# Kernel optimization log

Hardware: AMD Instinct MI355X
Metric: run time of the kernel (lower is better)

Reference implementation:

```python
import jax, jax.numpy as jnp
import numpy as np

N_U, N_I, D_IN_U, D_IN_I, D, D_QOL, B = 4096, 4096, 256, 256, 256, 4, 8192

def _w(key, shape, scale=0.05):
    return (jax.random.normal(key, shape) * scale).astype(jnp.float32)

def setup_inputs() -> dict:
    key = jax.random.key(0)
    ks = jax.random.split(key, 24)
    inp = {
        "x_u": jax.random.normal(ks[0], (N_U, D_IN_U), jnp.float32),
        "x_i": jax.random.normal(ks[1], (N_I, D_IN_I), jnp.float32),
        "social_adj": jax.random.randint(ks[2], (N_U, N_U), 0, 2, jnp.int32),
        "ui_adj": jax.random.randint(ks[3], (N_U, N_I), 0, 2, jnp.int32),
        "user_idx": jax.random.randint(ks[4], (B,), 0, N_U, jnp.int32),
        "item_idx": jax.random.randint(ks[5], (B,), 0, N_I, jnp.int32),
        "q_u": jax.random.normal(ks[6], (N_U, D_QOL), jnp.float32),
        # params (Linear stored as [in, out]; y = x @ W + b)
        "user_W": _w(ks[7], (D_IN_U, D)), "user_b": jnp.zeros((D,), jnp.float32),
        "item_W": _w(ks[8], (D_IN_I, D)), "item_b": jnp.zeros((D,), jnp.float32),
        "soc_W": _w(ks[9], (D, D)), "soc_a": _w(ks[10], (2 * D,)),
        "cnt_W": _w(ks[11], (D, D)), "cnt_a": _w(ks[12], (2 * D,)),
        "gate_W": _w(ks[13], (D_QOL, D)), "gate_b": jnp.zeros((D,), jnp.float32),
        "qproj_W": _w(ks[14], (D_QOL, D)), "qproj_b": jnp.zeros((D,), jnp.float32),
        "alpha_q": jnp.float32(0.3),
        "pred_W1": _w(ks[15], (2 * D, D)), "pred_b1": jnp.zeros((D,), jnp.float32),
        "pred_W2": _w(ks[16], (D, 1)), "pred_b2": jnp.zeros((1,), jnp.float32),
    }
    return inp

def _gat(Wh_src, Wh_dst, a, adj):
    """GAT additive attention: src rows attend over dst cols where adj!=0.
    Rows with no neighbors produce zero output (matches nan_to_num + zeroing)."""
    d = Wh_src.shape[-1]
    a1 = Wh_src @ a[:d]          # [N_src]
    a2 = Wh_dst @ a[d:]          # [N_dst]
    e = jax.nn.leaky_relu(a1[:, None] + a2[None, :], 0.2)  # [N_src, N_dst]
    mask = adj != 0
    neg_inf = jnp.float32(-jnp.inf)
    m = jnp.max(jnp.where(mask, e, neg_inf), axis=-1, keepdims=True)
    m = jnp.where(jnp.isfinite(m), m, 0.0)  # guard empty rows
    ex = jnp.where(mask, jnp.exp(e - m), 0.0)
    denom = jnp.sum(ex, axis=-1, keepdims=True)
    alpha = jnp.where(denom > 0, ex / jnp.where(denom > 0, denom, 1.0), 0.0)
    out = alpha @ Wh_dst
    return out, alpha

def reference(x_u, x_i, social_adj, ui_adj, user_idx, item_idx, q_u,
              user_W, user_b, item_W, item_b, soc_W, soc_a, cnt_W, cnt_a,
              gate_W, gate_b, qproj_W, qproj_b, alpha_q,
              pred_W1, pred_b1, pred_W2, pred_b2):
    h_u = x_u @ user_W + user_b               # [N_u, D]
    h_i = x_i @ item_W + item_b               # [N_i, D]
    # social attention (users over users)
    Wh = h_u @ soc_W
    soc_msg, alpha_s = _gat(Wh, Wh, soc_a, social_adj)
    # content attention (users over items)
    Wu = h_u @ cnt_W
    Wi = h_i @ cnt_W
    cnt_msg, alpha_c = _gat(Wu, Wi, cnt_a, ui_adj)
    h_u_out = jax.nn.elu(soc_msg + cnt_msg + h_u)
    # QoL gate
    gate = jax.nn.sigmoid(q_u @ gate_W + gate_b)
    qproj = q_u @ qproj_W + qproj_b
    h_u_out = h_u_out + alpha_q * gate * qproj
    # pair prediction (dropout inactive at eval)
    cat = jnp.concatenate([h_u_out[user_idx], h_i[item_idx]], axis=-1)  # [B, 2D]
    hid = jax.nn.relu(cat @ pred_W1 + pred_b1)
    r = (hid @ pred_W2 + pred_b2)[..., 0]
    r_hat = 1.0 + 4.0 * jax.nn.sigmoid(r)
    return r_hat, alpha_s, alpha_c
```

## Files before the change

### kernel.cpp

```cpp
#include <hip/hip_runtime.h>

typedef unsigned short u16;
typedef unsigned int u32;
typedef unsigned char u8;
typedef unsigned long long u64;
typedef float f32x4 __attribute__((ext_vector_type(4)));
typedef __bf16 bf16x8 __attribute__((ext_vector_type(8)));

#define NU 4096
#define DD 256
#define BB 8192

__device__ inline u16 f2b(float f) {
    u32 u = __builtin_bit_cast(u32, f);
    u32 r = (u + 0x7fffu + ((u >> 16) & 1u)) >> 16;
    return (u16)r;
}
__device__ inline float b2f(u16 v) { return __builtin_bit_cast(float, (u32)v << 16); }
__device__ inline float lrelu(float x) { return x > 0.f ? x : 0.2f * x; }
__device__ inline float decmax(u32 e) {
    return __builtin_bit_cast(float, (e >> 31) ? (e & 0x7fffffffu) : ~e);
}

#define BARRIER_LGKM() asm volatile("s_waitcnt lgkmcnt(0)\ns_barrier" ::: "memory")

__global__ __launch_bounds__(256) void k_pro(
    const float* __restrict__ x_u, const float* __restrict__ x_i,
    const float* __restrict__ user_W, const float* __restrict__ item_W, const float* __restrict__ pred_W1,
    const float* __restrict__ soc_W, const float* __restrict__ soc_a,
    const float* __restrict__ cnt_W, const float* __restrict__ cnt_a,
    const float* __restrict__ user_b, const float* __restrict__ item_b,
    u16* __restrict__ xu_b, u16* __restrict__ xi_b,
    u16* __restrict__ uWt, u16* __restrict__ iWt, u16* __restrict__ p1Wt,
    float* __restrict__ uvec,
    u16* __restrict__ WusT, u16* __restrict__ WicT,
    float* __restrict__ b_us, float* __restrict__ b_ic, u32* __restrict__ MhEnc) {
    __shared__ float t[64][65];
    __shared__ float sa[256];
    const int b = blockIdx.x;
    const int tid = threadIdx.x;

    if (b < 1024) {
        const float* in = (b < 512) ? x_u : x_i;
        u16* out = (b < 512) ? xu_b : xi_b;
        int i = (b & 511) * 256 + tid;
        const float4 v0 = *(const float4*)(in + (size_t)i * 8);
        const float4 v1 = *(const float4*)(in + (size_t)i * 8 + 4);
        u16 u[8] = {f2b(v0.x), f2b(v0.y), f2b(v0.z), f2b(v0.w),
                    f2b(v1.x), f2b(v1.y), f2b(v1.z), f2b(v1.w)};
        *(uint4*)(out + (size_t)i * 8) = *(uint4*)u;
    } else if (b < 1088) {
        int j = b - 1024;
        const float* in;
        u16* out;
        int R;
        if (j < 16) { in = user_W; out = uWt; R = 256; }
        else if (j < 32) { in = item_W; out = iWt; R = 256; j -= 16; }
        else { in = pred_W1; out = p1Wt; R = 512; j -= 32; }
        int rb = (j >> 2) * 64, cb = (j & 3) * 64;
        for (int k = 0; k < 16; ++k) {
            int idx = k * 256 + tid;
            int lr = idx >> 6, lc = idx & 63;
            t[lr][lc] = in[(size_t)(rb + lr) * 256 + cb + lc];
        }
        __syncthreads();
        for (int k = 0; k < 16; ++k) {
            int idx = k * 256 + tid;
            int lr = idx >> 6, lc = idx & 63;
            out[(size_t)(cb + lr) * R + rb + lc] = f2b(t[lc][lr]);
        }
    } else if (b < 1092) {
        int bb = b - 1088;
        if (bb == 0 && tid < 2) MhEnc[tid] = 0u;
        const float* W = (bb < 2) ? soc_W : cnt_W;
        const float* a = ((bb < 2) ? soc_a : cnt_a) + (bb & 1) * 256;
        int lane = tid & 63, wv = tid >> 6;
        sa[tid] = a[tid];
        __syncthreads();
        for (int rr = 0; rr < 64; ++rr) {
            int in = wv * 64 + rr;
            float4 w4 = *(const float4*)(W + (size_t)in * 256 + lane * 4);
            float acc = w4.x * sa[lane * 4] + w4.y * sa[lane * 4 + 1] + w4.z * sa[lane * 4 + 2] + w4.w * sa[lane * 4 + 3];
#pragma unroll
            for (int off = 32; off; off >>= 1) acc += __shfl_down(acc, off);
            if (lane == 0) uvec[bb * 256 + in] = acc;
        }
    } else {
        int j = b - 1092;
        int p = j >> 4;
        int tile = j & 15;
        const float* A = p ? item_W : user_W;
        const float* Bw = p ? cnt_W : soc_W;
        const float* bvec = p ? item_b : user_b;
        u16* outT = p ? WicT : WusT;
        float* outb = p ? b_ic : b_us;
        int m0 = (tile >> 2) * 64, n0 = (tile & 3) * 64;
        int m = m0 + (tid >> 4) * 4, n = n0 + (tid & 15) * 4;
        float acc[4][4];
#pragma unroll
        for (int i = 0; i < 4; ++i)
#pragma unroll
            for (int k = 0; k < 4; ++k) acc[i][k] = 0.f;
        for (int k0 = 0; k0 < 256; k0 += 4) {
            float aa[4][4], bb2[4][4];
#pragma unroll
            for (int i = 0; i < 4; ++i) {
                float4 v = *(const float4*)(A + (size_t)(m + i) * 256 + k0);
                aa[i][0] = v.x; aa[i][1] = v.y; aa[i][2] = v.z; aa[i][3] = v.w;
            }
#pragma unroll
            for (int k = 0; k < 4; ++k) {
                float4 v = *(const float4*)(Bw + (size_t)(k0 + k) * 256 + n);
                bb2[k][0] = v.x; bb2[k][1] = v.y; bb2[k][2] = v.z; bb2[k][3] = v.w;
            }
#pragma unroll
            for (int i = 0; i < 4; ++i)
#pragma unroll
                for (int k = 0; k < 4; ++k)
#pragma unroll
                    for (int jj = 0; jj < 4; ++jj) acc[i][jj] += aa[i][k] * bb2[k][jj];
        }
#pragma unroll
        for (int i = 0; i < 4; ++i)
#pragma unroll
            for (int jj = 0; jj < 4; ++jj) outT[(size_t)(n + jj) * 256 + m + i] = f2b(acc[i][jj]);
        if (tile >> 2 == 0 && tid < 64) {
            int nn = n0 + tid;
            float s = 0.f;
            for (int k = 0; k < 256; ++k) s += bvec[k] * Bw[(size_t)k * 256 + nn];
            outb[nn] = s;
        }
    }
}

__global__ __launch_bounds__(256) void k_gemm4(
    const u16* __restrict__ xu_b, const u16* __restrict__ xi_b,
    const u16* __restrict__ uWt, const u16* __restrict__ iWt,
    const u16* __restrict__ WusT, const u16* __restrict__ WicT,
    const float* __restrict__ user_b, const float* __restrict__ item_b,
    const float* __restrict__ b_us, const float* __restrict__ b_ic,
    float* __restrict__ h_u_f, float* __restrict__ h_i_f, u16* __restrict__ h_i_b,
    u16* __restrict__ WhT, u16* __restrict__ WiT) {
    const int z = blockIdx.z;
    const int M = 4096, N = 256, K = 256;
    const u16* A = (z == 0 || z == 2) ? xu_b : xi_b;
    const u16* Bt = (z == 0) ? uWt : (z == 1) ? iWt : (z == 2) ? WusT : WicT;
    const float* bias = (z == 0) ? user_b : (z == 1) ? item_b : (z == 2) ? b_us : b_ic;
    float* Cf = (z == 0) ? h_u_f : (z == 1) ? h_i_f : nullptr;
    u16* Cb = (z == 1) ? h_i_b : nullptr;
    u16* Cbt = (z == 2) ? WhT : (z == 3) ? WiT : nullptr;

    __shared__ u16 As[64 * 64];
    __shared__ u16 Bs[64 * 64];
    const int tid = threadIdx.x;
    const int lane = tid & 63, wv = tid >> 6;
    const int bm = blockIdx.x * 64, bn = blockIdx.y * 64;
    const int wm = (wv >> 1) * 32, wn = (wv & 1) * 32;
    f32x4 acc[2][2];
#pragma unroll
    for (int i = 0; i < 2; i++)
#pragma unroll
        for (int j = 0; j < 2; j++) acc[i][j] = f32x4{0.f, 0.f, 0.f, 0.f};

    char* Ab = (char*)As;
    char* Bb = (char*)Bs;
    const int r = tid >> 2;
    const int ib0 = (tid & 3) * 32;
    const int swz = (r & 7) << 4;

    for (int k0 = 0; k0 < K; k0 += 64) {
        const uint4* ga = (const uint4*)(A + (size_t)(bm + r) * K + k0 + (ib0 >> 1));
        const uint4* gb = (const uint4*)(Bt + (size_t)(bn + r) * K + k0 + (ib0 >> 1));
        uint4 va0 = ga[0], va1 = ga[1];
        uint4 vb0 = gb[0], vb1 = gb[1];
        __syncthreads();
        *(uint4*)(Ab + r * 128 + ((ib0) ^ swz)) = va0;
        *(uint4*)(Ab + r * 128 + ((ib0 + 16) ^ swz)) = va1;
        *(uint4*)(Bb + r * 128 + ((ib0) ^ swz)) = vb0;
        *(uint4*)(Bb + r * 128 + ((ib0 + 16) ^ swz)) = vb1;
        __syncthreads();
#pragma unroll
        for (int kh = 0; kh < 2; ++kh) {
            bf16x8 af[2], bfr[2];
#pragma unroll
            for (int mf = 0; mf < 2; ++mf) {
                int row = wm + mf * 16 + (lane & 15);
                int kb = kh * 64 + ((lane >> 4) << 4);
                af[mf] = *(const bf16x8*)(Ab + row * 128 + (kb ^ ((row & 7) << 4)));
            }
#pragma unroll
            for (int nf = 0; nf < 2; ++nf) {
                int row = wn + nf * 16 + (lane & 15);
                int kb = kh * 64 + ((lane >> 4) << 4);
                bfr[nf] = *(const bf16x8*)(Bb + row * 128 + (kb ^ ((row & 7) << 4)));
            }
#pragma unroll
            for (int mf = 0; mf < 2; ++mf)
#pragma unroll
                for (int nf = 0; nf < 2; ++nf)
                    acc[mf][nf] = __builtin_amdgcn_mfma_f32_16x16x32_bf16(af[mf], bfr[nf], acc[mf][nf], 0, 0, 0);
        }
    }
#pragma unroll
    for (int mf = 0; mf < 2; ++mf) {
#pragma unroll
        for (int nf = 0; nf < 2; ++nf) {
            int col = bn + wn + nf * 16 + (lane & 15);
            int row0 = bm + wm + mf * 16 + ((lane >> 4) << 2);
            float bv = bias[col];
            float v[4];
#pragma unroll
            for (int q = 0; q < 4; ++q) {
                float x = acc[mf][nf][q] + bv;
                v[q] = x;
                if (Cf) Cf[(size_t)(row0 + q) * N + col] = x;
                if (Cb) Cb[(size_t)(row0 + q) * N + col] = f2b(x);
            }
            if (Cbt) {
                uint2 p;
                p.x = (u32)f2b(v[0]) | ((u32)f2b(v[1]) << 16);
                p.y = (u32)f2b(v[2]) | ((u32)f2b(v[3]) << 16);
                *(uint2*)(Cbt + (size_t)col * M + row0) = p;
            }
        }
    }
}

__global__ __launch_bounds__(256) void k_gemv_a(const float* __restrict__ h_u, const float* __restrict__ h_i,
                                                const float* __restrict__ uvec, float* __restrict__ avec,
                                                u32* __restrict__ MhEnc) {
    int tid = threadIdx.x, lane = tid & 63, wv = tid >> 6;
    int ib = blockIdx.x * 64;
    const float* H = (wv == 3) ? h_i : h_u;
    const float* u = uvec + wv * 256;
    float4 u4 = *(const float4*)(u + lane * 4);
    float runm = -1e30f;
    for (int rr = 0; rr < 64; ++rr) {
        int row = ib + rr;
        float4 h4 = *(const float4*)(H + (size_t)row * 256 + lane * 4);
        float acc = h4.x * u4.x + h4.y * u4.y + h4.z * u4.z + h4.w * u4.w;
#pragma unroll
        for (int off = 32; off; off >>= 1) acc += __shfl_down(acc, off);
        if (lane == 0) {
            avec[wv * 4096 + row] = acc;
            runm = fmaxf(runm, acc);
        }
    }
    if (lane == 0 && (wv & 1)) {
        u32 b = __builtin_bit_cast(u32, runm);
        u32 e = (b >> 31) ? ~b : (b | 0x80000000u);
        atomicMax(&MhEnc[wv >> 1], e);
    }
}

__global__ __launch_bounds__(512, 4) void k_scanpv(const int* __restrict__ adjS, const int* __restrict__ adjC,
                                                   const float* __restrict__ avec, const u32* __restrict__ MhEnc,
                                                   const u16* __restrict__ WhT, const u16* __restrict__ WiT,
                                                   float* __restrict__ dpart, u8* __restrict__ bits,
                                                   u16* __restrict__ msgpart) {
    const int z = blockIdx.z;
    const int ib = blockIdx.x * 64;
    const int jb = blockIdx.y * 512;
    const int tid = threadIdx.x, lane = tid & 63, wv = tid >> 6;
    const int* adj = z ? adjC : adjS;
    const float* a1 = avec + z * 8192;
    const float* a2 = a1 + 4096;
    const u16* Pt = z ? WiT : WhT;
    u8* bz = bits + (size_t)z * 2097152;

    __shared__ float a2s[512];
    __shared__ float s_a1[64], s_mr[64];
    __shared__ u16 Atile[64 * 512];
    char* Ab = (char*)Atile;

    if (tid < 512) a2s[tid] = a2[jb + tid];
    if (tid < 64) {
        float a = a1[ib + tid];
        float mhg = decmax(MhEnc[z]);
        s_a1[tid] = a;
        s_mr[tid] = lrelu(a + mhg);
    }
    __syncthreads();

    const int r0 = wv * 8;
    const int boff = (jb >> 3) + lane;
    const float4 A0 = *(const float4*)(a2s + lane * 8);
    const float4 A1 = *(const float4*)(a2s + lane * 8 + 4);
    const float av[8] = {A0.x, A0.y, A0.z, A0.w, A1.x, A1.y, A1.z, A1.w};
#pragma unroll
    for (int rr = 0; rr < 8; ++rr) {
        const int r = r0 + rr;
        const int row = ib + r;
        const int4* p = (const int4*)(adj + (size_t)row * 4096 + jb + lane * 8);
        int4 v0 = p[0], v1 = p[1];
        const float a1r = s_a1[r], mr = s_mr[r];
        u32 bbyte = (u32)(v0.x != 0) | ((u32)(v0.y != 0) << 1) | ((u32)(v0.z != 0) << 2) | ((u32)(v0.w != 0) << 3) |
                    ((u32)(v1.x != 0) << 4) | ((u32)(v1.y != 0) << 5) | ((u32)(v1.z != 0) << 6) | ((u32)(v1.w != 0) << 7);
        bz[(size_t)row * 512 + boff] = (u8)bbyte;
        float ex[8];
        float acc = 0.f;
#pragma unroll
        for (int k = 0; k < 8; ++k) {
            float e = __expf(lrelu(a1r + av[k]) - mr);
            ex[k] = ((bbyte >> k) & 1) ? e : 0.f;
            acc += ex[k];
        }
#pragma unroll
        for (int off = 32; off; off >>= 1) acc += __shfl_down(acc, off);
        if (lane == 0) dpart[((size_t)z * 8 + blockIdx.y) * 4096 + row] = acc;
        u16 pk[8];
#pragma unroll
        for (int k = 0; k < 8; ++k) pk[k] = f2b(ex[k]);
        *(uint4*)(Ab + r * 1024 + ((lane * 16) ^ ((r & 7) << 4))) = *(uint4*)pk;
    }
    BARRIER_LGKM();

    f32x4 acc[4][2];
#pragma unroll
    for (int i = 0; i < 4; i++)
#pragma unroll
        for (int j = 0; j < 2; j++) acc[i][j] = f32x4{0.f, 0.f, 0.f, 0.f};

    const u16* pts = Pt + (size_t)(wv * 32 + (lane & 15)) * 4096 + jb + ((lane >> 4) << 3);
    bf16x8 bcur0 = *(const bf16x8*)(pts);
    bf16x8 bcur1 = *(const bf16x8*)(pts + (size_t)16 * 4096);
    for (int ks = 0; ks < 16; ++ks) {
        bf16x8 bnxt0, bnxt1;
        if (ks < 15) {
            bnxt0 = *(const bf16x8*)(pts + (ks + 1) * 32);
            bnxt1 = *(const bf16x8*)(pts + (size_t)16 * 4096 + (ks + 1) * 32);
        }
#pragma unroll
        for (int mf = 0; mf < 4; ++mf) {
            int ra = mf * 16 + (lane & 15);
            bf16x8 af = *(const bf16x8*)(Ab + ra * 1024 + ((ks * 64 + ((lane >> 4) << 4)) ^ ((ra & 7) << 4)));
            acc[mf][0] = __builtin_amdgcn_mfma_f32_16x16x32_bf16(af, bcur0, acc[mf][0], 0, 0, 0);
            acc[mf][1] = __builtin_amdgcn_mfma_f32_16x16x32_bf16(af, bcur1, acc[mf][1], 0, 0, 0);
        }
        bcur0 = bnxt0;
        bcur1 = bnxt1;
    }

    u16* mp = msgpart + ((size_t)(z * 8 + blockIdx.y) * 4096 + ib) * 256;
#pragma unroll
    for (int mf = 0; mf < 4; ++mf) {
        int rr = mf * 16 + ((lane >> 4) << 2);
#pragma unroll
        for (int nf = 0; nf < 2; ++nf) {
            int col = wv * 32 + nf * 16 + (lane & 15);
#pragma unroll
            for (int q = 0; q < 4; ++q) mp[(size_t)(rr + q) * 256 + col] = f2b(acc[mf][nf][q]);
        }
    }
}

__global__ __launch_bounds__(256) void k_alpha(const u8* __restrict__ bits,
                                               const float* __restrict__ avec, const u32* __restrict__ MhEnc,
                                               const float* __restrict__ dpart, float* __restrict__ out) {
    const int z = blockIdx.z;
    const int ib = blockIdx.x * 64;
    const int jb = blockIdx.y * 512;
    const int tid = threadIdx.x, lane = tid & 63, wv = tid >> 6;
    const u8* bz = bits + (size_t)z * 2097152;
    const float* a1 = avec + z * 8192;
    const float* a2 = a1 + 4096;
    float* alpha = out + 8192 + (size_t)z * 16777216;

    __shared__ float s_a1[64], s_mr[64], s_inv[64];
    if (tid < 64) {
        float a = a1[ib + tid];
        float mhg = decmax(MhEnc[z]);
        s_a1[tid] = a;
        s_mr[tid] = lrelu(a + mhg);
        float d = 0.f;
#pragma unroll
        for (int s = 0; s < 8; ++s) d += dpart[((size_t)(z * 8 + s)) * 4096 + ib + tid];
        s_inv[tid] = d > 0.f ? 1.f / d : 0.f;
    }
    const float4 A0 = *(const float4*)(a2 + jb + lane * 4);
    const float4 A1 = *(const float4*)(a2 + jb + 256 + lane * 4);
    const float av0[4] = {A0.x, A0.y, A0.z, A0.w};
    const float av1[4] = {A1.x, A1.y, A1.z, A1.w};
    __syncthreads();

    const int bb0 = (jb >> 3) + (lane >> 1);
    const int sh = (lane & 1) * 4;
    for (int rr = 0; rr < 16; ++rr) {
        const int r = wv * 16 + rr;
        const int row = ib + r;
        const float a1r = s_a1[r], mr = s_mr[r], ivr = s_inv[r];
        const u32 n0 = (u32)(bz[(size_t)row * 512 + bb0]) >> sh;
        const u32 n1 = (u32)(bz[(size_t)row * 512 + bb0 + 32]) >> sh;
        float o0[4], o1[4];
#pragma unroll
        for (int k = 0; k < 4; ++k) {
            o0[k] = ((n0 >> k) & 1) ? __expf(lrelu(a1r + av0[k]) - mr) * ivr : 0.f;
            o1[k] = ((n1 >> k) & 1) ? __expf(lrelu(a1r + av1[k]) - mr) * ivr : 0.f;
        }
        float* ap = alpha + (size_t)row * 4096 + jb;
        *(float4*)(ap + lane * 4) = float4{o0[0], o0[1], o0[2], o0[3]};
        *(float4*)(ap + 256 + lane * 4) = float4{o1[0], o1[1], o1[2], o1[3]};
    }
}

__global__ __launch_bounds__(256) void k_post(const u16* __restrict__ msgpart, const float* __restrict__ dpart,
                                              const float* __restrict__ h_u, const float* __restrict__ q_u,
                                              const float* __restrict__ gate_W, const float* __restrict__ gate_b,
                                              const float* __restrict__ qproj_W, const float* __restrict__ qproj_b,
                                              const float* __restrict__ alpha_q, u16* __restrict__ huo_b) {
    int i = blockIdx.x;
    int n = threadIdx.x;
    __shared__ float red[16];
    if (n < 16) red[n] = dpart[(size_t)n * 4096 + i];
    __syncthreads();
    float d0 = 0.f, d1 = 0.f;
#pragma unroll
    for (int p = 0; p < 8; ++p) { d0 += red[p]; d1 += red[8 + p]; }
    float inv0 = d0 > 0.f ? 1.f / d0 : 0.f;
    float inv1 = d1 > 0.f ? 1.f / d1 : 0.f;
    float s0 = 0.f, s1 = 0.f;
#pragma unroll
    for (int p = 0; p < 8; ++p) {
        s0 += b2f(msgpart[((size_t)p * 4096 + i) * 256 + n]);
        s1 += b2f(msgpart[((size_t)(8 + p) * 4096 + i) * 256 + n]);
    }
    float v = inv0 * s0 + inv1 * s1 + h_u[(size_t)i * 256 + n];
    v = v > 0.f ? v : expm1f(v);
    float q0 = q_u[i * 4 + 0], q1 = q_u[i * 4 + 1], q2 = q_u[i * 4 + 2], q3 = q_u[i * 4 + 3];
    float g = q0 * gate_W[n] + q1 * gate_W[256 + n] + q2 * gate_W[512 + n] + q3 * gate_W[768 + n] + gate_b[n];
    g = 1.f / (1.f + __expf(-g));
    float qp = q0 * qproj_W[n] + q1 * qproj_W[256 + n] + q2 * qproj_W[512 + n] + q3 * qproj_W[768 + n] + qproj_b[n];
    float o = v + alpha_q[0] * g * qp;
    huo_b[(size_t)i * 256 + n] = f2b(o);
}

__global__ __launch_bounds__(512) void k_pred(const u16* __restrict__ huo_b, const u16* __restrict__ h_i_b,
                                              const int* __restrict__ uidx, const int* __restrict__ iidx,
                                              const u16* __restrict__ Bt, const float* __restrict__ b1,
                                              const float* __restrict__ W2, const float* __restrict__ b2,
                                              float* __restrict__ out) {
    __shared__ u16 As[64 * 512];
    __shared__ float redL[512];
    const int tid = threadIdx.x, lane = tid & 63, wv = tid >> 6;
    const int bm = blockIdx.x * 64;
    char* Ab = (char*)As;

    {
        const int r = tid >> 3;
        const int uix = uidx[bm + r], iix = iidx[bm + r];
        const int sswz = (r & 7) << 4;
#pragma unroll
        for (int c = 0; c < 8; ++c) {
            int e = c * 64 + (tid & 7) * 8;
            const u16* src = (e < 256) ? (huo_b + (size_t)uix * 256 + e) : (h_i_b + (size_t)iix * 256 + (e - 256));
            uint4 v = *(const uint4*)src;
            *(uint4*)(Ab + r * 1024 + ((e * 2) ^ sswz)) = v;
        }
    }
    __syncthreads();

    const int n0 = wv * 32;
    f32x4 acc[4][2];
#pragma unroll
    for (int i = 0; i < 4; i++)
#pragma unroll
        for (int j = 0; j < 2; j++) acc[i][j] = f32x4{0.f, 0.f, 0.f, 0.f};

    for (int ks = 0; ks < 16; ++ks) {
        bf16x8 bfr[2];
#pragma unroll
        for (int nf = 0; nf < 2; ++nf)
            bfr[nf] = *(const bf16x8*)(Bt + (size_t)(n0 + nf * 16 + (lane & 15)) * 512 + ks * 32 + ((lane >> 4) << 3));
#pragma unroll
        for (int mf = 0; mf < 4; ++mf) {
            int ra = mf * 16 + (lane & 15);
            bf16x8 af = *(const bf16x8*)(Ab + ra * 1024 + ((ks * 64 + ((lane >> 4) << 4)) ^ ((ra & 7) << 4)));
#pragma unroll
            for (int nf = 0; nf < 2; ++nf)
                acc[mf][nf] = __builtin_amdgcn_mfma_f32_16x16x32_bf16(af, bfr[nf], acc[mf][nf], 0, 0, 0);
        }
    }

    float b1v[2], w2v[2];
#pragma unroll
    for (int nf = 0; nf < 2; ++nf) {
        int col = n0 + nf * 16 + (lane & 15);
        b1v[nf] = b1[col];
        w2v[nf] = W2[col];
    }
#pragma unroll
    for (int mf = 0; mf < 4; ++mf) {
#pragma unroll
        for (int q = 0; q < 4; ++q) {
            float val = 0.f;
#pragma unroll
            for (int nf = 0; nf < 2; ++nf) val += fmaxf(acc[mf][nf][q] + b1v[nf], 0.f) * w2v[nf];
#pragma unroll
            for (int off = 1; off < 16; off <<= 1) val += __shfl_xor(val, off);
            if ((lane & 15) == 0) redL[wv * 64 + mf * 16 + ((lane >> 4) << 2) + q] = val;
        }
    }
    __syncthreads();
    if (tid < 64) {
        float r = b2[0];
#pragma unroll
        for (int w = 0; w < 8; ++w) r += redL[w * 64 + tid];
        out[bm + tid] = 1.f + 4.f / (1.f + __expf(-r));
    }
}

extern "C" void kernel_launch(void* const* d_in, const int* in_sizes, int n_in,
                              void* d_out, int out_size, void* d_ws, size_t ws_size,
                              hipStream_t stream) {
    const float* x_u = (const float*)d_in[0];
    const float* x_i = (const float*)d_in[1];
    const int* adjS = (const int*)d_in[2];
    const int* adjC = (const int*)d_in[3];
    const int* uidx = (const int*)d_in[4];
    const int* iidx = (const int*)d_in[5];
    const float* q_u = (const float*)d_in[6];
    const float* user_W = (const float*)d_in[7];
    const float* user_b = (const float*)d_in[8];
    const float* item_W = (const float*)d_in[9];
    const float* item_b = (const float*)d_in[10];
    const float* soc_W = (const float*)d_in[11];
    const float* soc_a = (const float*)d_in[12];
    const float* cnt_W = (const float*)d_in[13];
    const float* cnt_a = (const float*)d_in[14];
    const float* gate_W = (const float*)d_in[15];
    const float* gate_b = (const float*)d_in[16];
    const float* qproj_W = (const float*)d_in[17];
    const float* qproj_b = (const float*)d_in[18];
    const float* alpha_q = (const float*)d_in[19];
    const float* pred_W1 = (const float*)d_in[20];
    const float* pred_b1 = (const float*)d_in[21];
    const float* pred_W2 = (const float*)d_in[22];
    const float* pred_b2 = (const float*)d_in[23];
    float* out = (float*)d_out;

    char* w = (char*)d_ws;
    size_t off = 0;
    auto alloc = [&](size_t bytes) -> void* {
        void* p = w + off;
        off = (off + bytes + 255) & ~(size_t)255;
        return p;
    };
    u16* xu_b = (u16*)alloc((size_t)NU * DD * 2);
    u16* xi_b = (u16*)alloc((size_t)NU * DD * 2);
    u16* uWt = (u16*)alloc(256 * 256 * 2);
    u16* iWt = (u16*)alloc(256 * 256 * 2);
    u16* p1Wt = (u16*)alloc(512 * 256 * 2);
    u16* WusT = (u16*)alloc(256 * 256 * 2);
    u16* WicT = (u16*)alloc(256 * 256 * 2);
    float* b_us = (float*)alloc(256 * 4);
    float* b_ic = (float*)alloc(256 * 4);
    float* uvec = (float*)alloc(4 * 256 * 4);
    float* h_u_f = (float*)alloc((size_t)NU * DD * 4);
    float* h_i_f = (float*)alloc((size_t)NU * DD * 4);
    u16* h_i_b = (u16*)alloc((size_t)NU * DD * 2);
    u16* WhT = (u16*)alloc((size_t)NU * DD * 2);
    u16* WiT = (u16*)alloc((size_t)NU * DD * 2);
    float* avec = (float*)alloc(4 * 4096 * 4);
    u32* MhEnc = (u32*)alloc(2 * 4);
    float* dpart = (float*)alloc((size_t)2 * 8 * 4096 * 4);
    u8* bits = (u8*)alloc((size_t)2 * 2097152);
    u16* msgpart = (u16*)alloc((size_t)16 * 4096 * 256 * 2);
    u16* huo_b = (u16*)alloc((size_t)NU * DD * 2);
    (void)in_sizes; (void)n_in; (void)out_size; (void)ws_size;

    k_pro<<<1124, 256, 0, stream>>>(x_u, x_i, user_W, item_W, pred_W1, soc_W, soc_a, cnt_W, cnt_a,
                                    user_b, item_b, xu_b, xi_b, uWt, iWt, p1Wt, uvec, WusT, WicT,
                                    b_us, b_ic, MhEnc);
    k_gemm4<<<dim3(64, 4, 4), 256, 0, stream>>>(xu_b, xi_b, uWt, iWt, WusT, WicT, user_b, item_b, b_us, b_ic,
                                                h_u_f, h_i_f, h_i_b, WhT, WiT);
    k_gemv_a<<<64, 256, 0, stream>>>(h_u_f, h_i_f, uvec, avec, MhEnc);
    k_scanpv<<<dim3(64, 8, 2), 512, 0, stream>>>(adjS, adjC, avec, MhEnc, WhT, WiT, dpart, bits, msgpart);
    k_alpha<<<dim3(64, 8, 2), 256, 0, stream>>>(bits, avec, MhEnc, dpart, out);
    k_post<<<4096, 256, 0, stream>>>(msgpart, dpart, h_u_f, q_u, gate_W, gate_b, qproj_W, qproj_b, alpha_q, huo_b);
    k_pred<<<128, 512, 0, stream>>>(huo_b, h_i_b, uidx, iidx, p1Wt, pred_b1, pred_W2, pred_b2, out);
}
```

Before: 191.1 us.

## Split adjacency bit-packing out of fused scan+PV kernel into separate pass

Moves the int32 adjacency-to-bitmask packing into a new kernel, k_scan, which runs first and issues all eight row loads up front for memory-level parallelism. k_pv then reads packed bytes instead of the 128MB of int32 adjacency, so the MFMA-heavy kernel with 4-block occupancy no longer stalls on streaming loads. The cost is an extra launch and a write-then-read round trip of the 4MB bitmask. Total adjacency traffic stays the same, but it runs in a lightweight streaming kernel.

```diff
diff --git a/kernel.cpp b/kernel.cpp
--- a/kernel.cpp
+++ b/kernel.cpp
@@ -253,20 +253,43 @@
     }
 }
 
-__global__ __launch_bounds__(512, 4) void k_scanpv(const int* __restrict__ adjS, const int* __restrict__ adjC,
-                                                   const float* __restrict__ avec, const u32* __restrict__ MhEnc,
-                                                   const u16* __restrict__ WhT, const u16* __restrict__ WiT,
-                                                   float* __restrict__ dpart, u8* __restrict__ bits,
-                                                   u16* __restrict__ msgpart) {
+__global__ __launch_bounds__(256) void k_scan(const int* __restrict__ adjS, const int* __restrict__ adjC,
+                                              u8* __restrict__ bits) {
+    const int z = blockIdx.z;
+    const int* adj = z ? adjC : adjS;
+    u8* bz = bits + (size_t)z * 2097152;
+    const int ib = blockIdx.x * 32, jb = blockIdx.y * 512;
+    const int lane = threadIdx.x & 63, wv = threadIdx.x >> 6;
+    const int r0 = wv * 8;
+    const int* base = adj + (size_t)(ib + r0) * 4096 + jb + lane * 8;
+    int4 va[8], vb[8];
+#pragma unroll
+    for (int rr = 0; rr < 8; ++rr) {
+        va[rr] = *(const int4*)(base + (size_t)rr * 4096);
+        vb[rr] = *(const int4*)(base + (size_t)rr * 4096 + 4);
+    }
+    const size_t bo = (size_t)(ib + r0) * 512 + (jb >> 3) + lane;
+#pragma unroll
+    for (int rr = 0; rr < 8; ++rr) {
+        int4 v0 = va[rr], v1 = vb[rr];
+        u32 b = (u32)(v0.x != 0) | ((u32)(v0.y != 0) << 1) | ((u32)(v0.z != 0) << 2) | ((u32)(v0.w != 0) << 3) |
+                ((u32)(v1.x != 0) << 4) | ((u32)(v1.y != 0) << 5) | ((u32)(v1.z != 0) << 6) | ((u32)(v1.w != 0) << 7);
+        bz[bo + (size_t)rr * 512] = (u8)b;
+    }
+}
+
+__global__ __launch_bounds__(512, 4) void k_pv(const u8* __restrict__ bits,
+                                               const float* __restrict__ avec, const u32* __restrict__ MhEnc,
+                                               const u16* __restrict__ WhT, const u16* __restrict__ WiT,
+                                               float* __restrict__ dpart, u16* __restrict__ msgpart) {
     const int z = blockIdx.z;
     const int ib = blockIdx.x * 64;
     const int jb = blockIdx.y * 512;
     const int tid = threadIdx.x, lane = tid & 63, wv = tid >> 6;
-    const int* adj = z ? adjC : adjS;
+    const u8* bz = bits + (size_t)z * 2097152;
     const float* a1 = avec + z * 8192;
     const float* a2 = a1 + 4096;
     const u16* Pt = z ? WiT : WhT;
-    u8* bz = bits + (size_t)z * 2097152;
 
     __shared__ float a2s[512];
     __shared__ float s_a1[64], s_mr[64];
@@ -283,31 +306,29 @@
     __syncthreads();
 
     const int r0 = wv * 8;
-    const int boff = (jb >> 3) + lane;
+    u8 bvv[8];
+    const size_t bo = (size_t)(ib + r0) * 512 + (jb >> 3) + lane;
+#pragma unroll
+    for (int rr = 0; rr < 8; ++rr) bvv[rr] = bz[bo + (size_t)rr * 512];
     const float4 A0 = *(const float4*)(a2s + lane * 8);
     const float4 A1 = *(const float4*)(a2s + lane * 8 + 4);
     const float av[8] = {A0.x, A0.y, A0.z, A0.w, A1.x, A1.y, A1.z, A1.w};
 #pragma unroll
     for (int rr = 0; rr < 8; ++rr) {
         const int r = r0 + rr;
-        const int row = ib + r;
-        const int4* p = (const int4*)(adj + (size_t)row * 4096 + jb + lane * 8);
-        int4 v0 = p[0], v1 = p[1];
         const float a1r = s_a1[r], mr = s_mr[r];
-        u32 bbyte = (u32)(v0.x != 0) | ((u32)(v0.y != 0) << 1) | ((u32)(v0.z != 0) << 2) | ((u32)(v0.w != 0) << 3) |
-                    ((u32)(v1.x != 0) << 4) | ((u32)(v1.y != 0) << 5) | ((u32)(v1.z != 0) << 6) | ((u32)(v1.w != 0) << 7);
-        bz[(size_t)row * 512 + boff] = (u8)bbyte;
+        const u32 byte = bvv[rr];
         float ex[8];
         float acc = 0.f;
 #pragma unroll
         for (int k = 0; k < 8; ++k) {
             float e = __expf(lrelu(a1r + av[k]) - mr);
-            ex[k] = ((bbyte >> k) & 1) ? e : 0.f;
+            ex[k] = ((byte >> k) & 1) ? e : 0.f;
             acc += ex[k];
         }
 #pragma unroll
         for (int off = 32; off; off >>= 1) acc += __shfl_down(acc, off);
-        if (lane == 0) dpart[((size_t)z * 8 + blockIdx.y) * 4096 + row] = acc;
+        if (lane == 0) dpart[((size_t)z * 8 + blockIdx.y) * 4096 + ib + r] = acc;
         u16 pk[8];
 #pragma unroll
         for (int k = 0; k < 8; ++k) pk[k] = f2b(ex[k]);
@@ -568,13 +589,14 @@
     u16* huo_b = (u16*)alloc((size_t)NU * DD * 2);
     (void)in_sizes; (void)n_in; (void)out_size; (void)ws_size;
 
+    k_scan<<<dim3(128, 8, 2), 256, 0, stream>>>(adjS, adjC, bits);
     k_pro<<<1124, 256, 0, stream>>>(x_u, x_i, user_W, item_W, pred_W1, soc_W, soc_a, cnt_W, cnt_a,
                                     user_b, item_b, xu_b, xi_b, uWt, iWt, p1Wt, uvec, WusT, WicT,
                                     b_us, b_ic, MhEnc);
     k_gemm4<<<dim3(64, 4, 4), 256, 0, stream>>>(xu_b, xi_b, uWt, iWt, WusT, WicT, user_b, item_b, b_us, b_ic,
                                                 h_u_f, h_i_f, h_i_b, WhT, WiT);
     k_gemv_a<<<64, 256, 0, stream>>>(h_u_f, h_i_f, uvec, avec, MhEnc);
-    k_scanpv<<<dim3(64, 8, 2), 512, 0, stream>>>(adjS, adjC, avec, MhEnc, WhT, WiT, dpart, bits, msgpart);
+    k_pv<<<dim3(64, 8, 2), 512, 0, stream>>>(bits, avec, MhEnc, WhT, WiT, dpart, msgpart);
     k_alpha<<<dim3(64, 8, 2), 256, 0, stream>>>(bits, avec, MhEnc, dpart, out);
     k_post<<<4096, 256, 0, stream>>>(msgpart, dpart, h_u_f, q_u, gate_W, gate_b, qproj_W, qproj_b, alpha_q, huo_b);
     k_pred<<<128, 512, 0, stream>>>(huo_b, h_i_b, uidx, iidx, p1Wt, pred_b1, pred_W2, pred_b2, out);
```

New measurement: 205.5 us. +7.6%, slower.
